# Performance work log

Hardware: AMD Instinct MI355X
Metric: run time of the kernel (lower is better)

Reference implementation:

```python
import jax, jax.numpy as jnp
import numpy as np

NC = 4        # num_components
HEADS = 24
DH = 64
D = HEADS * DH  # 1536
EPS = 1e-8


def setup_inputs() -> dict:
    key = jax.random.key(0)
    ks = jax.random.split(key, 7)
    btc, S, E = 4, 4096, 154
    w = lambda k: jax.random.normal(k, (D, D), jnp.float32) * 0.02
    return {
        "hidden_states": jax.random.normal(ks[0], (btc, S, D), jnp.float32),
        "encoder_hidden_states": jax.random.normal(ks[1], (btc, E, D), jnp.float32),
        "temperature": jnp.ones((1,), jnp.float32),
        "Wq": w(ks[2]),
        "Wk": w(ks[3]),
        "Wv": w(ks[4]),
        "Wo": w(ks[5]),
        "bo": jnp.zeros((D,), jnp.float32),
        "pad_length": 154,
    }


def reference(hidden_states, encoder_hidden_states, temperature, Wq, Wk, Wv, Wo, bo, pad_length):
    btc, S, d = hidden_states.shape          # batch*components, latent seq, hidden
    E = encoder_hidden_states.shape[1]       # encoder seq (== pad_length)
    b = btc // NC
    scale = DH ** -0.5
    residual = hidden_states

    def heads(x, L):  # [btc, L, D] -> [btc, H, L, dh]
        return x.reshape(btc, L, HEADS, DH).transpose(0, 2, 1, 3)

    q = heads(hidden_states @ Wq.T, S)
    k = heads(encoder_hidden_states @ Wk.T, E)
    v = heads(encoder_hidden_states @ Wv.T, E)

    # pad tokens are zeros projected through the same k/v weights (no bias -> zeros)
    pad_h = jnp.zeros((btc, pad_length, d), hidden_states.dtype)
    k_pad = heads(pad_h @ Wk.T, pad_length)
    v_pad = heads(pad_h @ Wv.T, pad_length)

    scores = jnp.einsum('bhsd,bhed->bhse', q, k) / (temperature[0] + EPS)
    scores_pad = jnp.einsum('bhsd,bhpd->bhsp', q, k_pad) * scale

    # cross-component softmax over dim 0
    scores = scores.reshape(NC, b, HEADS, S, E)
    scores_pad = scores_pad.reshape(NC, b, HEADS, S, pad_length)
    w = jax.nn.softmax(scores, axis=0)
    w_pad = jax.nn.softmax(scores_pad, axis=0) * (NC / pad_length) * (1.0 - w)

    weights = jnp.concatenate(
        [w.reshape(btc, HEADS, S, E), w_pad.reshape(btc, HEADS, S, pad_length)],
        axis=-1)                              # [btc, H, S, E+pad]
    v_cat = jnp.concatenate([v, v_pad], axis=2)  # [btc, H, E+pad, dh]

    out = jnp.einsum('bhse,bhed->bhsd', weights, v_cat)
    out = out.transpose(0, 2, 1, 3).reshape(btc, S, d)
    out = out @ Wo.T + bo
    return out + residual
```

## Files before the change

kernel.cpp:

```cpp
#include <hip/hip_runtime.h>

typedef __attribute__((ext_vector_type(8))) short short8;
typedef __attribute__((ext_vector_type(4))) float f32x4;
typedef __attribute__((ext_vector_type(4))) unsigned short us4;
typedef __attribute__((ext_vector_type(4))) float float4v;

#define GLB_PTR(p) ((const __attribute__((address_space(1))) void*)(p))
#define LDS_PTR(p) ((__attribute__((address_space(3))) void*)(p))

__device__ __forceinline__ unsigned short f2bf(float f) {
  unsigned int u = __float_as_uint(f);
  u += 0x7FFF + ((u >> 16) & 1);
  return (unsigned short)(u >> 16);
}

__global__ void cvt_all(const float* __restrict__ i0, const float* __restrict__ i1,
                        const float* __restrict__ i2, const float* __restrict__ i3,
                        const float* __restrict__ i4, const float* __restrict__ i5,
                        unsigned short* __restrict__ o0, unsigned short* __restrict__ o1,
                        unsigned short* __restrict__ o2, unsigned short* __restrict__ o3,
                        unsigned short* __restrict__ o4, unsigned short* __restrict__ o5) {
  constexpr int N0 = 16384 * 1536 / 4, N1 = 616 * 1536 / 4, NW = 1536 * 1536 / 4;
  constexpr int TOT = N0 + N1 + 4 * NW;
  int i = blockIdx.x * blockDim.x + threadIdx.x;
  const int stride = gridDim.x * blockDim.x;
  for (; i < TOT; i += stride) {
    const float* in; unsigned short* out; int j = i;
    if (j < N0)              { in = i0; out = o0; }
    else if ((j -= N0) < N1) { in = i1; out = o1; }
    else {
      j -= N1;
      const int t = j / NW; j -= t * NW;
      in  = t == 0 ? i2 : t == 1 ? i3 : t == 2 ? i4 : i5;
      out = t == 0 ? o2 : t == 1 ? o3 : t == 2 ? o4 : o5;
    }
    float4v v = *(const float4v*)(in + (size_t)j * 4);
    us4 o;
    o[0] = f2bf(v[0]); o[1] = f2bf(v[1]); o[2] = f2bf(v[2]); o[3] = f2bf(v[3]);
    *(us4*)(out + (size_t)j * 4) = o;
  }
}

template<int MODE>
__device__ __forceinline__ void gemm_big_body(
    const unsigned short* __restrict__ A,
    const unsigned short* __restrict__ B,
    unsigned short* __restrict__ Cb,
    float* __restrict__ Cf,
    const float* __restrict__ bias,
    const float* __restrict__ resid,
    unsigned short* smem, int bid, int tid) {
  constexpr int K = 1536, N = 1536, BK = 32, NKT = K / BK;
  unsigned short* As = smem;
  unsigned short* Bs = smem + 2 * 8192;

  const int xcd = bid & 7, idx = bid >> 3;
  const int m0 = (xcd * 8 + idx / 12) * 256;
  const int n0 = (idx % 12) * 128;

  const int w = tid >> 6, l = tid & 63, lr = l & 15, lg = l >> 4;
  const int wr = w >> 1, wc = w & 1;
  const int ga = lg ^ ((lr >> 1) & 3);

  const int srow = tid >> 2;
  const int sg = (l & 3) ^ ((l >> 3) & 3);
  const unsigned short* aSrc = A + (size_t)(m0 + srow) * K + sg * 8;
  const unsigned short* bSrc = B + (size_t)(n0 + srow) * K + sg * 8;

  f32x4 acc[8][4] = {};

  auto stage = [&](int buf, int kt) {
    const int k0 = kt * BK;
    unsigned short* AsW = As + buf * 8192 + w * 512;
    unsigned short* BsW = Bs + buf * 4096 + w * 512;
#pragma unroll
    for (int i = 0; i < 4; ++i)
      __builtin_amdgcn_global_load_lds(GLB_PTR(aSrc + (size_t)(i * 64) * K + k0), LDS_PTR(AsW + i * 2048), 16, 0, 0);
#pragma unroll
    for (int i = 0; i < 2; ++i)
      __builtin_amdgcn_global_load_lds(GLB_PTR(bSrc + (size_t)(i * 64) * K + k0), LDS_PTR(BsW + i * 2048), 16, 0, 0);
  };

  auto loadfrags = [&](int buf, short8* af, short8* bfv) {
    const unsigned short* Asb = As + buf * 8192;
    const unsigned short* Bsb = Bs + buf * 4096;
#pragma unroll
    for (int i = 0; i < 8; ++i)
      af[i] = *(const short8*)(Asb + (wr * 128 + i * 16 + lr) * 32 + ga * 8);
#pragma unroll
    for (int j = 0; j < 4; ++j)
      bfv[j] = *(const short8*)(Bsb + (wc * 64 + j * 16 + lr) * 32 + ga * 8);
  };

  auto mfma_all = [&](short8* af, short8* bfv) {
#pragma unroll
    for (int i = 0; i < 8; ++i)
#pragma unroll
      for (int j = 0; j < 4; ++j)
        acc[i][j] = __builtin_amdgcn_mfma_f32_16x16x32_bf16(af[i], bfv[j], acc[i][j], 0, 0, 0);
  };

  stage(0, 0); stage(1, 1);

  for (int kt = 0; kt < NKT; ++kt) {
    if (kt < NKT - 1) asm volatile("s_waitcnt vmcnt(6)" ::: "memory");
    else              asm volatile("s_waitcnt vmcnt(0)" ::: "memory");
    __builtin_amdgcn_s_barrier();
    __builtin_amdgcn_sched_barrier(0);
    short8 af[8], bfv[4];
    loadfrags(kt & 1, af, bfv);
    asm volatile("s_waitcnt lgkmcnt(0)" ::: "memory");
    __builtin_amdgcn_sched_barrier(0);
    __builtin_amdgcn_s_barrier();
    __builtin_amdgcn_sched_barrier(0);
    if (kt + 2 < NKT) stage(kt & 1, kt + 2);
    __builtin_amdgcn_s_setprio(1);
    mfma_all(af, bfv);
    __builtin_amdgcn_s_setprio(0);
  }

#pragma unroll
  for (int i = 0; i < 8; ++i) {
    const int rb = m0 + wr * 128 + i * 16 + lg * 4;
#pragma unroll
    for (int j = 0; j < 4; ++j) {
      const int col = n0 + wc * 64 + j * 16 + lr;
#pragma unroll
      for (int r = 0; r < 4; ++r) {
        size_t o = (size_t)(rb + r) * N + col;
        if (MODE == 0) Cb[o] = f2bf(acc[i][j][r]);
        else           Cf[o] = acc[i][j][r] + bias[col] + resid[o];
      }
    }
  }
}

__device__ __forceinline__ void gemm_kv_body(
    const unsigned short* __restrict__ A,
    const unsigned short* __restrict__ Bk,
    const unsigned short* __restrict__ Bv,
    unsigned short* __restrict__ Ck,
    unsigned short* __restrict__ Vt,
    unsigned short* smem, int by, int tid) {
  constexpr int K = 1536, N = 1536, Mc = 615;
  unsigned short* As = smem;
  unsigned short* Bs = smem + 4096;
  const int bx = by % 5, yy = by / 5;
  const unsigned short* B = yy < 12 ? Bk : Bv;
  const int m0 = bx * 128, n0 = (yy % 12) * 128;
  const int t = tid;
  const int w = t >> 6, l = t & 63, lr = l & 15, lg = l >> 4;
  const int wr = w >> 1, wc = w & 1;
  const int srow = t >> 2, scol = (t & 3) * 8;

  f32x4 acc[4][4] = {};
  unsigned short* AsW = As + w * 512;
  unsigned short* BsW = Bs + w * 512;
  long ar0 = m0 + srow;       if (ar0 > Mc) ar0 = Mc;
  long ar1 = m0 + srow + 64;  if (ar1 > Mc) ar1 = Mc;

  for (int k0 = 0; k0 < K; k0 += 32) {
    __builtin_amdgcn_global_load_lds(GLB_PTR(A + ar0 * (long)K + k0 + scol), LDS_PTR(AsW),        16, 0, 0);
    __builtin_amdgcn_global_load_lds(GLB_PTR(A + ar1 * (long)K + k0 + scol), LDS_PTR(AsW + 2048), 16, 0, 0);
    __builtin_amdgcn_global_load_lds(GLB_PTR(B + (long)(n0 + srow) * K + k0 + scol),      LDS_PTR(BsW),        16, 0, 0);
    __builtin_amdgcn_global_load_lds(GLB_PTR(B + (long)(n0 + srow + 64) * K + k0 + scol), LDS_PTR(BsW + 2048), 16, 0, 0);
    __syncthreads();

    short8 af[4], bfv[4];
#pragma unroll
    for (int i = 0; i < 4; ++i) {
      af[i]  = *(const short8*)(As + (wr * 64 + i * 16 + lr) * 32 + lg * 8);
      bfv[i] = *(const short8*)(Bs + (wc * 64 + i * 16 + lr) * 32 + lg * 8);
    }
#pragma unroll
    for (int i = 0; i < 4; ++i)
#pragma unroll
      for (int j = 0; j < 4; ++j)
        acc[i][j] = __builtin_amdgcn_mfma_f32_16x16x32_bf16(af[i], bfv[j], acc[i][j], 0, 0, 0);
    __syncthreads();
  }

  if (yy < 12) {
#pragma unroll
    for (int i = 0; i < 4; ++i) {
      int rb = m0 + wr * 64 + i * 16 + lg * 4;
#pragma unroll
      for (int j = 0; j < 4; ++j) {
        int col = n0 + wc * 64 + j * 16 + lr;
#pragma unroll
        for (int r = 0; r < 4; ++r)
          Ck[(long)(rb + r) * N + col] = f2bf(acc[i][j][r]);
      }
    }
  } else {
#pragma unroll
    for (int i = 0; i < 4; ++i) {
      int rb = m0 + wr * 64 + i * 16 + lg * 4;
#pragma unroll
      for (int j = 0; j < 4; ++j) {
        int col = n0 + wc * 64 + j * 16 + lr;
        int hh = col >> 6, dd = col & 63;
#pragma unroll
        for (int r = 0; r < 4; ++r) {
          int m = rb + r;
          if (m < 616) {
            int c = (unsigned)m / 154u;
            int e = m - c * 154;
            Vt[((long)((c * 24 + hh) * 64 + dd)) * 160 + e] = f2bf(acc[i][j][r]);
          }
        }
      }
    }
  }
}

__global__ __launch_bounds__(256, 2) void gemm_q_kv(
    const unsigned short* __restrict__ HSb, const unsigned short* __restrict__ Wqb,
    unsigned short* __restrict__ Qb,
    const unsigned short* __restrict__ EHSb, const unsigned short* __restrict__ Wkb,
    const unsigned short* __restrict__ Wvb,
    unsigned short* __restrict__ Ck, unsigned short* __restrict__ Vt) {
  __shared__ unsigned short smem[24576];
  if (blockIdx.x < 768)
    gemm_big_body<0>(HSb, Wqb, Qb, nullptr, nullptr, nullptr, smem, blockIdx.x, threadIdx.x);
  else
    gemm_kv_body(EHSb, Wkb, Wvb, Ck, Vt, smem, blockIdx.x - 768, threadIdx.x);
}

__global__ __launch_bounds__(256, 2) void gemm_o(
    const unsigned short* __restrict__ Ob, const unsigned short* __restrict__ Wob,
    float* __restrict__ Cf, const float* __restrict__ bias, const float* __restrict__ resid) {
  __shared__ unsigned short smem[24576];
  gemm_big_body<1>(Ob, Wob, nullptr, Cf, bias, resid, smem, blockIdx.x, threadIdx.x);
}

__global__ __launch_bounds__(256) void attn_kernel(
    const unsigned short* __restrict__ Qb,
    const unsigned short* __restrict__ Kb,
    const unsigned short* __restrict__ Vt,
    const float* __restrict__ temp,
    unsigned short* __restrict__ Ob) {
  __shared__ unsigned short P[4][4][16][160];
  const int h = blockIdx.y, sb = blockIdx.x;
  const int t = threadIdx.x, w = t >> 6, l = t & 63, lr = l & 15, lg = l >> 4;
  const int s0 = sb * 64 + w * 16;
  const float sc = 1.0f / (temp[0] + 1e-8f);

  short8 qf[4][2];
#pragma unroll
  for (int c = 0; c < 4; ++c)
#pragma unroll
    for (int kt = 0; kt < 2; ++kt)
      qf[c][kt] = *(const short8*)(Qb + (long)(c * 4096 + s0 + lr) * 1536 + h * 64 + kt * 32 + lg * 8);

  short8 kA[4][2], kB[4][2];
  auto loadK = [&](int et, short8 (&k)[4][2]) {
#pragma unroll
    for (int c = 0; c < 4; ++c)
#pragma unroll
      for (int kt = 0; kt < 2; ++kt)
        k[c][kt] = *(const short8*)(Kb + (long)(c * 154 + et * 16 + lr) * 1536 + h * 64 + kt * 32 + lg * 8);
  };

  auto qk_step = [&](int et, short8 (&kc)[4][2], short8 (&kn)[4][2], bool pre) {
    if (pre) loadK(et + 1, kn);
    f32x4 sa[4] = {};
#pragma unroll
    for (int c = 0; c < 4; ++c)
#pragma unroll
      for (int kt = 0; kt < 2; ++kt)
        sa[c] = __builtin_amdgcn_mfma_f32_16x16x32_bf16(kc[c][kt], qf[c][kt], sa[c], 0, 0, 0);
    float wv[4][4];
#pragma unroll
    for (int r = 0; r < 4; ++r) {
      float e0 = __expf(sa[0][r] * sc), e1 = __expf(sa[1][r] * sc);
      float e2 = __expf(sa[2][r] * sc), e3 = __expf(sa[3][r] * sc);
      float inv = 1.0f / (e0 + e1 + e2 + e3);
      wv[0][r] = e0 * inv; wv[1][r] = e1 * inv; wv[2][r] = e2 * inv; wv[3][r] = e3 * inv;
    }
#pragma unroll
    for (int c = 0; c < 4; ++c) {
      us4 pk;
#pragma unroll
      for (int r = 0; r < 4; ++r)
        pk[r] = (et * 16 + lg * 4 + r < 154) ? f2bf(wv[c][r]) : (unsigned short)0;
      *(us4*)&P[w][c][lr][et * 16 + lg * 4] = pk;
    }
  };

  loadK(0, kA);
#pragma unroll
  for (int et = 0; et < 10; et += 2) {
    qk_step(et,     kA, kB, true);
    qk_step(et + 1, kB, kA, et + 1 < 9);
  }
  asm volatile("s_waitcnt lgkmcnt(0)" ::: "memory");
  __builtin_amdgcn_sched_barrier(0);

  short8 vA[4], vB[4];
  auto loadV = [&](int c, int ks, short8 (&v)[4]) {
#pragma unroll
    for (int nt = 0; nt < 4; ++nt)
      v[nt] = *(const short8*)(Vt + (long)((c * 24 + h) * 64 + nt * 16 + lr) * 160 + ks * 32 + lg * 8);
  };

  f32x4 o[4][4] = {};
  loadV(0, 0, vA);
#pragma unroll
  for (int p = 0; p < 10; ++p) {
    const int i0 = 2 * p, i1 = 2 * p + 1;
    const int c0 = i0 / 5, k0 = i0 % 5;
    const int c1 = i1 / 5, k1 = i1 % 5;
    loadV(c1, k1, vB);
    short8 pf0 = *(const short8*)&P[w][c0][lr][k0 * 32 + lg * 8];
#pragma unroll
    for (int nt = 0; nt < 4; ++nt)
      o[c0][nt] = __builtin_amdgcn_mfma_f32_16x16x32_bf16(pf0, vA[nt], o[c0][nt], 0, 0, 0);
    if (p < 9) loadV((i1 + 1) / 5, (i1 + 1) % 5, vA);
    short8 pf1 = *(const short8*)&P[w][c1][lr][k1 * 32 + lg * 8];
#pragma unroll
    for (int nt = 0; nt < 4; ++nt)
      o[c1][nt] = __builtin_amdgcn_mfma_f32_16x16x32_bf16(pf1, vB[nt], o[c1][nt], 0, 0, 0);
  }

  unsigned short* OS = &P[w][0][0][0];
#pragma unroll
  for (int c = 0; c < 4; ++c) {
#pragma unroll
    for (int nt = 0; nt < 4; ++nt)
#pragma unroll
      for (int r = 0; r < 4; ++r)
        OS[(lg * 4 + r) * 64 + nt * 16 + lr] = f2bf(o[c][nt][r]);
    asm volatile("s_waitcnt lgkmcnt(0)" ::: "memory");
    __builtin_amdgcn_sched_barrier(0);
#pragma unroll
    for (int p = 0; p < 2; ++p) {
      const int flat = p * 512 + l * 8;
      const int row = flat >> 6, col = flat & 63;
      short8 v = *(const short8*)(OS + flat);
      *(short8*)(Ob + (long)(c * 4096 + s0 + row) * 1536 + h * 64 + col) = v;
    }
  }
}

extern "C" void kernel_launch(void* const* d_in, const int* in_sizes, int n_in,
                              void* d_out, int out_size, void* d_ws, size_t ws_size,
                              hipStream_t stream) {
  (void)in_sizes; (void)n_in; (void)out_size; (void)ws_size;
  const float* HS  = (const float*)d_in[0];
  const float* EHS = (const float*)d_in[1];
  const float* TMP = (const float*)d_in[2];
  const float* Wq  = (const float*)d_in[3];
  const float* Wk  = (const float*)d_in[4];
  const float* Wv  = (const float*)d_in[5];
  const float* Wo  = (const float*)d_in[6];
  const float* bo  = (const float*)d_in[7];

  char* ws = (char*)d_ws;
  size_t off = 0;
  unsigned short* HSb  = (unsigned short*)(ws + off); off += (size_t)16384 * 1536 * 2;
  unsigned short* Ob   = HSb;
  unsigned short* EHSb = (unsigned short*)(ws + off); off += (size_t)616 * 1536 * 2;
  unsigned short* Wqb  = (unsigned short*)(ws + off); off += (size_t)1536 * 1536 * 2;
  unsigned short* Wkb  = (unsigned short*)(ws + off); off += (size_t)1536 * 1536 * 2;
  unsigned short* Wvb  = (unsigned short*)(ws + off); off += (size_t)1536 * 1536 * 2;
  unsigned short* Wob  = (unsigned short*)(ws + off); off += (size_t)1536 * 1536 * 2;
  unsigned short* Kb   = (unsigned short*)(ws + off); off += (size_t)640 * 1536 * 2;
  unsigned short* Vt   = (unsigned short*)(ws + off); off += (size_t)4 * 24 * 64 * 160 * 2;
  unsigned short* Qb   = (unsigned short*)d_out;

  cvt_all<<<2048, 256, 0, stream>>>(HS, EHS, Wq, Wk, Wv, Wo,
                                    HSb, EHSb, Wqb, Wkb, Wvb, Wob);

  gemm_q_kv<<<888, 256, 0, stream>>>(HSb, Wqb, Qb, EHSb, Wkb, Wvb, Kb, Vt);

  attn_kernel<<<dim3(64, 24), 256, 0, stream>>>(Qb, Kb, Vt, TMP, Ob);

  gemm_o<<<768, 256, 0, stream>>>(Ob, Wob, (float*)d_out, bo, HS);
}
```

Before: 337.9 us.

## Interleave QK softmax and PV accumulation per key chunk to shrink LDS

The attention kernel now computes scores and cross-component softmax for one 32-key chunk, then immediately runs the PV MFMAs for that chunk, instead of materialising the full 160-key probability tile first. This shrinks the per-block shared buffer from about 80 KB to about 16 KB, which allows more resident blocks per CU, and it lets V loads overlap with QK work. The cost is a wait on LDS each chunk and a tighter interleaving that may reduce ILP within a wave. Each wave writes and reads only its own slice, so no block barrier is needed.

```diff
diff --git a/kernel.cpp b/kernel.cpp
--- a/kernel.cpp
+++ b/kernel.cpp
@@ -240,7 +240,7 @@
     const unsigned short* __restrict__ Vt,
     const float* __restrict__ temp,
     unsigned short* __restrict__ Ob) {
-  __shared__ unsigned short P[4][4][16][160];
+  __shared__ unsigned short P2[4][4][16][32];
   const int h = blockIdx.y, sb = blockIdx.x;
   const int t = threadIdx.x, w = t >> 6, l = t & 63, lr = l & 15, lg = l >> 4;
   const int s0 = sb * 64 + w * 16;
@@ -278,24 +278,16 @@
       float inv = 1.0f / (e0 + e1 + e2 + e3);
       wv[0][r] = e0 * inv; wv[1][r] = e1 * inv; wv[2][r] = e2 * inv; wv[3][r] = e3 * inv;
     }
+    const int el = (et & 1) * 16 + lg * 4;
 #pragma unroll
     for (int c = 0; c < 4; ++c) {
       us4 pk;
 #pragma unroll
       for (int r = 0; r < 4; ++r)
         pk[r] = (et * 16 + lg * 4 + r < 154) ? f2bf(wv[c][r]) : (unsigned short)0;
-      *(us4*)&P[w][c][lr][et * 16 + lg * 4] = pk;
-    }
-  };
-
-  loadK(0, kA);
-#pragma unroll
-  for (int et = 0; et < 10; et += 2) {
-    qk_step(et,     kA, kB, true);
-    qk_step(et + 1, kB, kA, et + 1 < 9);
-  }
-  asm volatile("s_waitcnt lgkmcnt(0)" ::: "memory");
-  __builtin_amdgcn_sched_barrier(0);
+      *(us4*)&P2[w][c][lr][el] = pk;
+    }
+  };
 
   short8 vA[4], vB[4];
   auto loadV = [&](int c, int ks, short8 (&v)[4]) {
@@ -305,25 +297,29 @@
   };
 
   f32x4 o[4][4] = {};
+  loadK(0, kA);
   loadV(0, 0, vA);
 #pragma unroll
-  for (int p = 0; p < 10; ++p) {
-    const int i0 = 2 * p, i1 = 2 * p + 1;
-    const int c0 = i0 / 5, k0 = i0 % 5;
-    const int c1 = i1 / 5, k1 = i1 % 5;
-    loadV(c1, k1, vB);
-    short8 pf0 = *(const short8*)&P[w][c0][lr][k0 * 32 + lg * 8];
-#pragma unroll
-    for (int nt = 0; nt < 4; ++nt)
-      o[c0][nt] = __builtin_amdgcn_mfma_f32_16x16x32_bf16(pf0, vA[nt], o[c0][nt], 0, 0, 0);
-    if (p < 9) loadV((i1 + 1) / 5, (i1 + 1) % 5, vA);
-    short8 pf1 = *(const short8*)&P[w][c1][lr][k1 * 32 + lg * 8];
-#pragma unroll
-    for (int nt = 0; nt < 4; ++nt)
-      o[c1][nt] = __builtin_amdgcn_mfma_f32_16x16x32_bf16(pf1, vB[nt], o[c1][nt], 0, 0, 0);
-  }
-
-  unsigned short* OS = &P[w][0][0][0];
+  for (int ks = 0; ks < 5; ++ks) {
+    qk_step(2 * ks,     kA, kB, true);
+    qk_step(2 * ks + 1, kB, kA, ks < 4);
+    asm volatile("s_waitcnt lgkmcnt(0)" ::: "memory");
+    __builtin_amdgcn_sched_barrier(0);
+#pragma unroll
+    for (int c = 0; c < 4; ++c) {
+      if (c == 0)      loadV(1, ks, vB);
+      else if (c == 1) loadV(2, ks, vA);
+      else if (c == 2) loadV(3, ks, vB);
+      else if (ks < 4) loadV(0, ks + 1, vA);
+      short8 pf = *(const short8*)&P2[w][c][lr][lg * 8];
+      short8* vv = (c & 1) ? vB : vA;
+#pragma unroll
+      for (int nt = 0; nt < 4; ++nt)
+        o[c][nt] = __builtin_amdgcn_mfma_f32_16x16x32_bf16(pf, vv[nt], o[c][nt], 0, 0, 0);
+    }
+  }
+
+  unsigned short* OS = &P2[w][0][0][0];
 #pragma unroll
   for (int c = 0; c < 4; ++c) {
 #pragma unroll
```

After: 345.6 us. 2.3% more time.

## Fuse hidden_states fp32-to-bf16 conversion into Q projection GEMM

Applied to the files above, without the earlier changes.

The Q projection GEMM now reads fp32 hidden_states directly, converting to bf16 in registers before writing to LDS. This removes the separate 16384x1536 conversion pass and its bf16 round trip through memory. The Q GEMM block moves to 512 threads with a 256x128 tile and 4x4 accumulators per wave, a reworked register-staged pipeline, and a 4-blocks-per-CU launch bound. The KV GEMM path leaves its upper 256 threads idle. It reads twice the A bytes from global memory and adds VALU conversion work inside the main loop.

```diff
diff --git a/kernel.cpp b/kernel.cpp
--- a/kernel.cpp
+++ b/kernel.cpp
@@ -14,20 +14,19 @@
   return (unsigned short)(u >> 16);
 }
 
-__global__ void cvt_all(const float* __restrict__ i0, const float* __restrict__ i1,
+__global__ void cvt_all(const float* __restrict__ i1,
                         const float* __restrict__ i2, const float* __restrict__ i3,
                         const float* __restrict__ i4, const float* __restrict__ i5,
-                        unsigned short* __restrict__ o0, unsigned short* __restrict__ o1,
+                        unsigned short* __restrict__ o1,
                         unsigned short* __restrict__ o2, unsigned short* __restrict__ o3,
                         unsigned short* __restrict__ o4, unsigned short* __restrict__ o5) {
-  constexpr int N0 = 16384 * 1536 / 4, N1 = 616 * 1536 / 4, NW = 1536 * 1536 / 4;
-  constexpr int TOT = N0 + N1 + 4 * NW;
+  constexpr int N1 = 616 * 1536 / 4, NW = 1536 * 1536 / 4;
+  constexpr int TOT = N1 + 4 * NW;
   int i = blockIdx.x * blockDim.x + threadIdx.x;
   const int stride = gridDim.x * blockDim.x;
   for (; i < TOT; i += stride) {
     const float* in; unsigned short* out; int j = i;
-    if (j < N0)              { in = i0; out = o0; }
-    else if ((j -= N0) < N1) { in = i1; out = o1; }
+    if (j < N1) { in = i1; out = o1; }
     else {
       j -= N1;
       const int t = j / NW; j -= t * NW;
@@ -41,11 +40,114 @@
   }
 }
 
-template<int MODE>
-__device__ __forceinline__ void gemm_big_body(
+__device__ __forceinline__ void gemm_q_body(
+    const float* __restrict__ A,
+    const unsigned short* __restrict__ B,
+    unsigned short* __restrict__ Cb,
+    unsigned short* smem, int bid, int tid) {
+  constexpr int K = 1536, N = 1536, BK = 32, NKT = K / BK;
+  unsigned short* As = smem;
+  unsigned short* Bs = smem + 2 * 8192;
+
+  const int xcd = bid & 7, idx = bid >> 3;
+  const int m0 = (xcd * 8 + idx / 12) * 256;
+  const int n0 = (idx % 12) * 128;
+
+  const int w = tid >> 6, l = tid & 63, lr = l & 15, lg = l >> 4;
+  const int wr = w >> 1, wc = w & 1;
+  const int ga = lg ^ ((lr >> 1) & 3);
+
+  const int srow = w * 16 + (l >> 2);
+  const int sg = (l & 3) ^ ((l >> 3) & 3);
+  const float* aSrc0 = A + (size_t)(m0 + srow) * K + sg * 8;
+  const float* aSrc1 = A + (size_t)(m0 + 128 + srow) * K + sg * 8;
+  const unsigned short* bSrc = B + (size_t)(n0 + srow) * K + sg * 8;
+
+  f32x4 acc[4][4] = {};
+  float4v aR[2][2];
+
+  auto issueA = [&](int kt) {
+    if (kt >= NKT) return;
+    const int k0 = kt * BK;
+    aR[0][0] = *(const float4v*)(aSrc0 + k0);
+    aR[0][1] = *(const float4v*)(aSrc0 + k0 + 4);
+    aR[1][0] = *(const float4v*)(aSrc1 + k0);
+    aR[1][1] = *(const float4v*)(aSrc1 + k0 + 4);
+  };
+  auto cvtwrite = [&](int buf) {
+#pragma unroll
+    for (int i = 0; i < 2; ++i) {
+      short8 v;
+#pragma unroll
+      for (int e = 0; e < 4; ++e) {
+        v[e]     = (short)f2bf(aR[i][0][e]);
+        v[e + 4] = (short)f2bf(aR[i][1][e]);
+      }
+      *(short8*)(&As[buf * 8192 + i * 4096 + w * 512 + l * 8]) = v;
+    }
+  };
+  auto stageB = [&](int buf, int kt) {
+    if (kt >= NKT) return;
+    __builtin_amdgcn_global_load_lds(GLB_PTR(bSrc + kt * BK),
+        LDS_PTR(Bs + buf * 4096 + w * 512), 16, 0, 0);
+  };
+  auto loadfrags = [&](int buf, short8* af, short8* bfv) {
+#pragma unroll
+    for (int i = 0; i < 4; ++i)
+      af[i] = *(const short8*)(&As[buf * 8192 + (wr * 64 + i * 16 + lr) * 32 + ga * 8]);
+#pragma unroll
+    for (int j = 0; j < 4; ++j)
+      bfv[j] = *(const short8*)(&Bs[buf * 4096 + (wc * 64 + j * 16 + lr) * 32 + ga * 8]);
+  };
+
+  issueA(0); stageB(0, 0);
+  asm volatile("s_waitcnt vmcnt(0)" ::: "memory");
+  cvtwrite(0);
+  issueA(1); stageB(1, 1);
+  asm volatile("s_waitcnt vmcnt(0)" ::: "memory");
+  cvtwrite(1);
+  issueA(2);
+  asm volatile("s_waitcnt lgkmcnt(0)" ::: "memory");
+  __builtin_amdgcn_s_barrier();
+
+  for (int kt = 0; kt < NKT; ++kt) {
+    short8 af[4], bfv[4];
+    loadfrags(kt & 1, af, bfv);
+    asm volatile("s_waitcnt lgkmcnt(0)" ::: "memory");
+    __builtin_amdgcn_sched_barrier(0);
+    __builtin_amdgcn_s_barrier();
+    __builtin_amdgcn_sched_barrier(0);
+    asm volatile("s_waitcnt vmcnt(0)" ::: "memory");
+    __builtin_amdgcn_sched_barrier(0);
+    if (kt + 2 < NKT) cvtwrite(kt & 1);
+    issueA(kt + 3);
+    stageB(kt & 1, kt + 2);
+    __builtin_amdgcn_s_setprio(1);
+#pragma unroll
+    for (int i = 0; i < 4; ++i)
+#pragma unroll
+      for (int j = 0; j < 4; ++j)
+        acc[i][j] = __builtin_amdgcn_mfma_f32_16x16x32_bf16(af[i], bfv[j], acc[i][j], 0, 0, 0);
+    __builtin_amdgcn_s_setprio(0);
+    __builtin_amdgcn_s_barrier();
+  }
+
+#pragma unroll
+  for (int i = 0; i < 4; ++i) {
+    const int rb = m0 + wr * 64 + i * 16 + lg * 4;
+#pragma unroll
+    for (int j = 0; j < 4; ++j) {
+      const int col = n0 + wc * 64 + j * 16 + lr;
+#pragma unroll
+      for (int r = 0; r < 4; ++r)
+        Cb[(size_t)(rb + r) * N + col] = f2bf(acc[i][j][r]);
+    }
+  }
+}
+
+__device__ __forceinline__ void gemm_o_body(
     const unsigned short* __restrict__ A,
     const unsigned short* __restrict__ B,
-    unsigned short* __restrict__ Cb,
     float* __restrict__ Cf,
     const float* __restrict__ bias,
     const float* __restrict__ resid,
@@ -92,14 +194,6 @@
       bfv[j] = *(const short8*)(Bsb + (wc * 64 + j * 16 + lr) * 32 + ga * 8);
   };
 
-  auto mfma_all = [&](short8* af, short8* bfv) {
-#pragma unroll
-    for (int i = 0; i < 8; ++i)
-#pragma unroll
-      for (int j = 0; j < 4; ++j)
-        acc[i][j] = __builtin_amdgcn_mfma_f32_16x16x32_bf16(af[i], bfv[j], acc[i][j], 0, 0, 0);
-  };
-
   stage(0, 0); stage(1, 1);
 
   for (int kt = 0; kt < NKT; ++kt) {
@@ -115,7 +209,11 @@
     __builtin_amdgcn_sched_barrier(0);
     if (kt + 2 < NKT) stage(kt & 1, kt + 2);
     __builtin_amdgcn_s_setprio(1);
-    mfma_all(af, bfv);
+#pragma unroll
+    for (int i = 0; i < 8; ++i)
+#pragma unroll
+      for (int j = 0; j < 4; ++j)
+        acc[i][j] = __builtin_amdgcn_mfma_f32_16x16x32_bf16(af[i], bfv[j], acc[i][j], 0, 0, 0);
     __builtin_amdgcn_s_setprio(0);
   }
 
@@ -128,8 +226,7 @@
 #pragma unroll
       for (int r = 0; r < 4; ++r) {
         size_t o = (size_t)(rb + r) * N + col;
-        if (MODE == 0) Cb[o] = f2bf(acc[i][j][r]);
-        else           Cf[o] = acc[i][j][r] + bias[col] + resid[o];
+        Cf[o] = acc[i][j][r] + bias[col] + resid[o];
       }
     }
   }
@@ -148,6 +245,7 @@
   const int bx = by % 5, yy = by / 5;
   const unsigned short* B = yy < 12 ? Bk : Bv;
   const int m0 = bx * 128, n0 = (yy % 12) * 128;
+  const bool act = tid < 256;
   const int t = tid;
   const int w = t >> 6, l = t & 63, lr = l & 15, lg = l >> 4;
   const int wr = w >> 1, wc = w & 1;
@@ -160,26 +258,30 @@
   long ar1 = m0 + srow + 64;  if (ar1 > Mc) ar1 = Mc;
 
   for (int k0 = 0; k0 < K; k0 += 32) {
-    __builtin_amdgcn_global_load_lds(GLB_PTR(A + ar0 * (long)K + k0 + scol), LDS_PTR(AsW),        16, 0, 0);
-    __builtin_amdgcn_global_load_lds(GLB_PTR(A + ar1 * (long)K + k0 + scol), LDS_PTR(AsW + 2048), 16, 0, 0);
-    __builtin_amdgcn_global_load_lds(GLB_PTR(B + (long)(n0 + srow) * K + k0 + scol),      LDS_PTR(BsW),        16, 0, 0);
-    __builtin_amdgcn_global_load_lds(GLB_PTR(B + (long)(n0 + srow + 64) * K + k0 + scol), LDS_PTR(BsW + 2048), 16, 0, 0);
+    if (act) {
+      __builtin_amdgcn_global_load_lds(GLB_PTR(A + ar0 * (long)K + k0 + scol), LDS_PTR(AsW),        16, 0, 0);
+      __builtin_amdgcn_global_load_lds(GLB_PTR(A + ar1 * (long)K + k0 + scol), LDS_PTR(AsW + 2048), 16, 0, 0);
+      __builtin_amdgcn_global_load_lds(GLB_PTR(B + (long)(n0 + srow) * K + k0 + scol),      LDS_PTR(BsW),        16, 0, 0);
+      __builtin_amdgcn_global_load_lds(GLB_PTR(B + (long)(n0 + srow + 64) * K + k0 + scol), LDS_PTR(BsW + 2048), 16, 0, 0);
+    }
     __syncthreads();
-
-    short8 af[4], bfv[4];
-#pragma unroll
-    for (int i = 0; i < 4; ++i) {
-      af[i]  = *(const short8*)(As + (wr * 64 + i * 16 + lr) * 32 + lg * 8);
-      bfv[i] = *(const short8*)(Bs + (wc * 64 + i * 16 + lr) * 32 + lg * 8);
-    }
-#pragma unroll
-    for (int i = 0; i < 4; ++i)
-#pragma unroll
-      for (int j = 0; j < 4; ++j)
-        acc[i][j] = __builtin_amdgcn_mfma_f32_16x16x32_bf16(af[i], bfv[j], acc[i][j], 0, 0, 0);
+    if (act) {
+      short8 af[4], bfv[4];
+#pragma unroll
+      for (int i = 0; i < 4; ++i) {
+        af[i]  = *(const short8*)(As + (wr * 64 + i * 16 + lr) * 32 + lg * 8);
+        bfv[i] = *(const short8*)(Bs + (wc * 64 + i * 16 + lr) * 32 + lg * 8);
+      }
+#pragma unroll
+      for (int i = 0; i < 4; ++i)
+#pragma unroll
+        for (int j = 0; j < 4; ++j)
+          acc[i][j] = __builtin_amdgcn_mfma_f32_16x16x32_bf16(af[i], bfv[j], acc[i][j], 0, 0, 0);
+    }
     __syncthreads();
   }
 
+  if (!act) return;
   if (yy < 12) {
 #pragma unroll
     for (int i = 0; i < 4; ++i) {
@@ -214,15 +316,15 @@
   }
 }
 
-__global__ __launch_bounds__(256, 2) void gemm_q_kv(
-    const unsigned short* __restrict__ HSb, const unsigned short* __restrict__ Wqb,
+__global__ __launch_bounds__(512, 4) void gemm_q_kv(
+    const float* __restrict__ HS, const unsigned short* __restrict__ Wqb,
     unsigned short* __restrict__ Qb,
     const unsigned short* __restrict__ EHSb, const unsigned short* __restrict__ Wkb,
     const unsigned short* __restrict__ Wvb,
     unsigned short* __restrict__ Ck, unsigned short* __restrict__ Vt) {
   __shared__ unsigned short smem[24576];
   if (blockIdx.x < 768)
-    gemm_big_body<0>(HSb, Wqb, Qb, nullptr, nullptr, nullptr, smem, blockIdx.x, threadIdx.x);
+    gemm_q_body(HS, Wqb, Qb, smem, blockIdx.x, threadIdx.x);
   else
     gemm_kv_body(EHSb, Wkb, Wvb, Ck, Vt, smem, blockIdx.x - 768, threadIdx.x);
 }
@@ -231,7 +333,7 @@
     const unsigned short* __restrict__ Ob, const unsigned short* __restrict__ Wob,
     float* __restrict__ Cf, const float* __restrict__ bias, const float* __restrict__ resid) {
   __shared__ unsigned short smem[24576];
-  gemm_big_body<1>(Ob, Wob, nullptr, Cf, bias, resid, smem, blockIdx.x, threadIdx.x);
+  gemm_o_body(Ob, Wob, Cf, bias, resid, smem, blockIdx.x, threadIdx.x);
 }
 
 __global__ __launch_bounds__(256) void attn_kernel(
@@ -358,8 +460,7 @@
 
   char* ws = (char*)d_ws;
   size_t off = 0;
-  unsigned short* HSb  = (unsigned short*)(ws + off); off += (size_t)16384 * 1536 * 2;
-  unsigned short* Ob   = HSb;
+  unsigned short* Ob   = (unsigned short*)(ws + off); off += (size_t)16384 * 1536 * 2;
   unsigned short* EHSb = (unsigned short*)(ws + off); off += (size_t)616 * 1536 * 2;
   unsigned short* Wqb  = (unsigned short*)(ws + off); off += (size_t)1536 * 1536 * 2;
   unsigned short* Wkb  = (unsigned short*)(ws + off); off += (size_t)1536 * 1536 * 2;
@@ -369,10 +470,10 @@
   unsigned short* Vt   = (unsigned short*)(ws + off); off += (size_t)4 * 24 * 64 * 160 * 2;
   unsigned short* Qb   = (unsigned short*)d_out;
 
-  cvt_all<<<2048, 256, 0, stream>>>(HS, EHS, Wq, Wk, Wv, Wo,
-                                    HSb, EHSb, Wqb, Wkb, Wvb, Wob);
-
-  gemm_q_kv<<<888, 256, 0, stream>>>(HSb, Wqb, Qb, EHSb, Wkb, Wvb, Kb, Vt);
+  cvt_all<<<1024, 256, 0, stream>>>(EHS, Wq, Wk, Wv, Wo,
+                                    EHSb, Wqb, Wkb, Wvb, Wob);
+
+  gemm_q_kv<<<888, 512, 0, stream>>>(HS, Wqb, Qb, EHSb, Wkb, Wvb, Kb, Vt);
 
   attn_kernel<<<dim3(64, 24), 256, 0, stream>>>(Qb, Kb, Vt, TMP, Ob);
 
```

Result: slower. 379.7 us (+12.4%).
